# Performance work log

Measured on AMD Instinct MI355X. Metric: run time of the kernel, lower is better.

Reference implementation:

```python
import jax, jax.numpy as jnp
import numpy as np

NUM_EXPERTS = 8
IN_FEATURES = 1024
HIDDEN_FEATURES = 4096
OUT_FEATURES = 1024
TOKENS = 8192


def setup_inputs() -> dict:
    key = jax.random.key(0)
    k_x, k_idx, k_w1, k_w2, k_b1, k_b2 = jax.random.split(key, 6)
    x = jax.random.normal(k_x, (TOKENS, IN_FEATURES), dtype=jnp.float32)
    indices_s = jax.random.randint(k_idx, (TOKENS,), 0, NUM_EXPERTS, dtype=jnp.int64)
    # learned parameters (torch uses torch.rand; scaled for numeric sanity)
    weight1 = jax.random.normal(k_w1, (NUM_EXPERTS, IN_FEATURES, HIDDEN_FEATURES), dtype=jnp.float32) * 0.02
    weight2 = jax.random.normal(k_w2, (NUM_EXPERTS, HIDDEN_FEATURES, OUT_FEATURES), dtype=jnp.float32) * 0.02
    bias1 = jax.random.normal(k_b1, (NUM_EXPERTS, HIDDEN_FEATURES), dtype=jnp.float32) * 0.02
    bias2 = jax.random.normal(k_b2, (NUM_EXPERTS, IN_FEATURES), dtype=jnp.float32) * 0.02
    return {"x": x, "indices_s": indices_s, "weight1": weight1, "weight2": weight2, "bias1": bias1, "bias2": bias2}


def reference(x, indices_s, weight1, weight2, bias1, bias2):
    # Per-token expert MLP. Rather than gathering full weight matrices per
    # token (weight[indices_s] -> [T, in, hid], huge), loop over the small
    # fixed expert set and mask-combine. Math identical to the torch module.
    T = x.shape[0]
    num_experts = weight1.shape[0]
    out = jnp.zeros((T, weight2.shape[2]), dtype=x.dtype)
    for e in range(num_experts):
        mask = (indices_s == e)[:, None]  # [T, 1]
        h = jax.nn.gelu(x @ weight1[e] + bias1[e], approximate=False)  # [T, hid]
        y = h @ weight2[e] + bias2[e]  # [T, out]
        out = out + jnp.where(mask, y, jnp.zeros((), dtype=x.dtype))
    # original returns shape [T, 1, out] (x was unsqueezed)
    return out[:, None, :]
```

## Files before the change

kernel.cpp:

```cpp
#include <hip/hip_runtime.h>
#include <hip/hip_bf16.h>
#include <math.h>

#define TOKENS 8192
#define IN_F   1024
#define HID_F  4096
#define OUT_F  1024
#define NEXP   8
#define TSLOTS 40

typedef __attribute__((ext_vector_type(8))) short bf16x8;
typedef __attribute__((ext_vector_type(4))) float f32x4;
typedef __attribute__((ext_vector_type(8))) unsigned short u16x8;

__device__ __forceinline__ unsigned short f2bf(float f) {
    unsigned int u = __float_as_uint(f);
    u += 0x7fffu + ((u >> 16) & 1u);
    return (unsigned short)(u >> 16);
}

__device__ __forceinline__ void gload_lds16(const unsigned short* g, unsigned char* lds) {
    __builtin_amdgcn_global_load_lds(
        (const __attribute__((address_space(1))) void*)g,
        (__attribute__((address_space(3))) void*)lds, 16, 0, 0);
}

__global__ void sort_kernel(const int* __restrict__ idx, int* __restrict__ perm,
                            int* __restrict__ off, int* __restrict__ table) {
    __shared__ int cnt[NEXP];
    __shared__ int base[NEXP];
    const int tid = threadIdx.x, lane = tid & 63;
    if (tid < NEXP) cnt[tid] = 0;
    __syncthreads();
    for (int i = tid; i < TOKENS; i += 1024) {
        int e = idx[i];
#pragma unroll
        for (int ex = 0; ex < NEXP; ++ex) {
            unsigned long long m = __ballot(e == ex);
            if (lane == 0 && m) atomicAdd(&cnt[ex], __popcll(m));
        }
    }
    __syncthreads();
    if (tid == 0) {
        int s = 0;
        for (int e = 0; e < NEXP; ++e) { off[e] = s; base[e] = s; s += cnt[e]; }
        off[NEXP] = s;
        int t = 0;
        for (int e = 0; e < NEXP; ++e)
            for (int m0 = off[e]; m0 < off[e + 1]; m0 += 256)
                table[t++] = (e << 13) | m0;
        for (; t < TSLOTS; ++t) table[t] = -1;
    }
    __syncthreads();
    for (int i = tid; i < TOKENS; i += 1024) {
        int e = idx[i];
#pragma unroll
        for (int ex = 0; ex < NEXP; ++ex) {
            unsigned long long m = __ballot(e == ex);
            if (e == ex) {
                int lead = (int)__ffsll((long long)m) - 1;
                int pos = 0;
                if (lane == lead) pos = atomicAdd(&base[ex], __popcll(m));
                pos = __shfl(pos, lead);
                pos += __popcll(m & ((1ULL << lane) - 1ULL));
                perm[pos] = i;
            }
        }
    }
}

__global__ void gather_x(const float* __restrict__ x, const int* __restrict__ perm,
                         unsigned short* __restrict__ xg) {
    const int row = blockIdx.x, t = threadIdx.x;
    const int src = perm[row];
    float4 v = *(const float4*)(x + (size_t)src * IN_F + t * 4);
    unsigned long long pk =
        (unsigned long long)f2bf(v.x) |
        ((unsigned long long)f2bf(v.y) << 16) |
        ((unsigned long long)f2bf(v.z) << 32) |
        ((unsigned long long)f2bf(v.w) << 48);
    *(unsigned long long*)(xg + (size_t)row * IN_F + t * 4) = pk;
}

__global__ void transp(const float* __restrict__ in, unsigned short* __restrict__ out,
                       int R, int C) {
    __shared__ unsigned short T[64 * 65];
    const int e = blockIdx.z;
    const int r0 = blockIdx.y * 64, c0 = blockIdx.x * 64;
    const int tid = threadIdx.x;
    const int rr = tid >> 4, cc = tid & 15;
    const float* ip = in + ((size_t)e * R + r0) * C + c0;
#pragma unroll
    for (int p = 0; p < 4; ++p) {
        int r = p * 16 + rr;
        float4 v = *(const float4*)(ip + (size_t)r * C + cc * 4);
        T[(cc * 4 + 0) * 65 + r] = f2bf(v.x);
        T[(cc * 4 + 1) * 65 + r] = f2bf(v.y);
        T[(cc * 4 + 2) * 65 + r] = f2bf(v.z);
        T[(cc * 4 + 3) * 65 + r] = f2bf(v.w);
    }
    __syncthreads();
    unsigned short* op = out + ((size_t)e * C + c0) * R + r0;
    const int c = tid >> 2, ch = tid & 3;
    u16x8 a, b;
#pragma unroll
    for (int i = 0; i < 8; ++i) a[i] = T[c * 65 + ch * 16 + i];
#pragma unroll
    for (int i = 0; i < 8; ++i) b[i] = T[c * 65 + ch * 16 + 8 + i];
    *(u16x8*)(op + (size_t)c * R + ch * 16) = a;
    *(u16x8*)(op + (size_t)c * R + ch * 16 + 8) = b;
}

#define RD_A(RB, HALF) \
  _Pragma("unroll") for (int m_ = 0; m_ < 4; ++m_) { \
    const int row_ = wr * 128 + (HALF) * 64 + m_ * 16 + lr; \
    _Pragma("unroll") for (int kk_ = 0; kk_ < 2; ++kk_) \
      aR[m_][kk_] = *(const bf16x8*)((RB) + row_ * 128 + (((kk_ * 4 + hk) << 4) ^ xorc)); }

#define RD_B(RB, NH, DST) \
  _Pragma("unroll") for (int nn_ = 0; nn_ < 2; ++nn_) { \
    const int row_ = wc * 64 + ((NH) * 2 + nn_) * 16 + lr; \
    _Pragma("unroll") for (int kk_ = 0; kk_ < 2; ++kk_) \
      DST[nn_][kk_] = *(const bf16x8*)((RB) + 32768 + row_ * 128 + (((kk_ * 4 + hk) << 4) ^ xorc)); }

#define MFMA_Q(MH, NH, B) \
  __builtin_amdgcn_s_setprio(1); \
  _Pragma("unroll") for (int m_ = 0; m_ < 4; ++m_) \
    _Pragma("unroll") for (int nn_ = 0; nn_ < 2; ++nn_) \
      _Pragma("unroll") for (int kk_ = 0; kk_ < 2; ++kk_) \
        acc[(MH) * 4 + m_][(NH) * 2 + nn_] = __builtin_amdgcn_mfma_f32_16x16x32_bf16( \
            aR[m_][kk_], B[nn_][kk_], acc[(MH) * 4 + m_][(NH) * 2 + nn_], 0, 0, 0); \
  __builtin_amdgcn_s_setprio(0);

template<int K, int ND, bool GELU>
__launch_bounds__(512, 2)
__global__ void moe_gemm8p(const unsigned short* __restrict__ A,
                           const unsigned short* __restrict__ W,
                           const float* __restrict__ bias,
                           const int* __restrict__ perm,
                           const int* __restrict__ off,
                           const int* __restrict__ table,
                           void* __restrict__ outp) {
    const int nwg = (ND / 256) * TSLOTS;
    const int chunk = nwg >> 3;
    const int logical = ((int)blockIdx.x & 7) * chunk + ((int)blockIdx.x >> 3);
    const int nt = logical / TSLOTS;
    const int ts = logical - nt * TSLOTS;
    const int te = table[ts];
    if (te < 0) return;
    const int e  = te >> 13;
    const int m0 = te & 8191;
    const int sege = off[e + 1];
    const int n0 = nt * 256;

    __shared__ __align__(16) unsigned char L[131072];

    const int tid = threadIdx.x;
    const int wid = tid >> 6, lane = tid & 63;
    const int wr = wid >> 2, wc = wid & 3;
    const int lr = lane & 15, hk = lane >> 4;

    const unsigned short* We = W + (size_t)e * ND * K + (size_t)n0 * K;

    const int srow8 = lane >> 3;
    const int sch   = (lane & 7) ^ srow8;
    const unsigned short* aSrc[4];
    const unsigned short* wSrc[4];
#pragma unroll
    for (int cc = 0; cc < 4; ++cc) {
        int rt = cc * 64 + wid * 8 + srow8;
        int ga = m0 + rt; if (ga > TOKENS - 1) ga = TOKENS - 1;
        aSrc[cc] = A  + (size_t)ga * K + sch * 8;
        wSrc[cc] = We + (size_t)rt * K + sch * 8;
    }
    const int dstBase = wid * 1024;

    constexpr int NT = K / 64;

    auto stageH = [&](int tile, int h) {
        const int buf = (tile & 1) * 65536;
        const int op  = (h >> 1) * 32768;
        const int c0_ = (h & 1) * 2;
        const int ko  = tile * 64;
#pragma unroll
        for (int j = 0; j < 2; ++j) {
            int cc = c0_ + j;
            const unsigned short* s = (h < 2) ? (aSrc[cc] + ko) : (wSrc[cc] + ko);
            gload_lds16(s, L + buf + op + cc * 8192 + dstBase);
        }
    };

    f32x4 acc[8][4];
#pragma unroll
    for (int i = 0; i < 8; ++i)
#pragma unroll
        for (int j = 0; j < 4; ++j) acc[i][j] = (f32x4){0.f, 0.f, 0.f, 0.f};

    bf16x8 aR[4][2], b0R[2][2], b1R[2][2];
    const int xorc = (lr & 7) << 4;
    const unsigned char* rb0 = L;
    const unsigned char* rb1 = L + 65536;

    stageH(0, 0); stageH(0, 1); stageH(0, 2); stageH(0, 3);
    stageH(1, 0);
    asm volatile("s_waitcnt vmcnt(2)" ::: "memory");
    __builtin_amdgcn_s_barrier();
    __builtin_amdgcn_sched_barrier(0);

#pragma unroll 1
    for (int i = 0; i < NT / 2; ++i) {
        const int T1 = 2 * i + 1;
        const bool lastIt = (i == NT / 2 - 1);
        RD_A(rb0, 0); RD_B(rb0, 0, b0R);
        stageH(T1, 1);
        __builtin_amdgcn_s_barrier();
        MFMA_Q(0, 0, b0R);
        __builtin_amdgcn_s_barrier();
        RD_B(rb0, 1, b1R);
        stageH(T1, 2);
        __builtin_amdgcn_s_barrier();
        MFMA_Q(0, 1, b1R);
        __builtin_amdgcn_s_barrier();
        RD_A(rb0, 1);
        stageH(T1, 3);
        __builtin_amdgcn_s_barrier();
        MFMA_Q(1, 1, b1R);
        __builtin_amdgcn_s_barrier();
        RD_B(rb0, 0, b0R);
        if (!lastIt) stageH(T1 + 1, 0);
        __builtin_amdgcn_s_barrier();
        MFMA_Q(1, 0, b0R);
        if (lastIt) { asm volatile("s_waitcnt vmcnt(0)" ::: "memory"); }
        else        { asm volatile("s_waitcnt vmcnt(2)" ::: "memory"); }
        __builtin_amdgcn_s_barrier();
        __builtin_amdgcn_sched_barrier(0);
        RD_A(rb1, 0); RD_B(rb1, 0, b0R);
        if (!lastIt) stageH(T1 + 1, 1);
        __builtin_amdgcn_s_barrier();
        MFMA_Q(0, 0, b0R);
        __builtin_amdgcn_s_barrier();
        RD_B(rb1, 1, b1R);
        if (!lastIt) stageH(T1 + 1, 2);
        __builtin_amdgcn_s_barrier();
        MFMA_Q(0, 1, b1R);
        __builtin_amdgcn_s_barrier();
        RD_A(rb1, 1);
        if (!lastIt) stageH(T1 + 1, 3);
        __builtin_amdgcn_s_barrier();
        MFMA_Q(1, 1, b1R);
        __builtin_amdgcn_s_barrier();
        RD_B(rb1, 0, b0R);
        if (!lastIt) stageH(T1 + 2, 0);
        __builtin_amdgcn_s_barrier();
        MFMA_Q(1, 0, b0R);
        if (!lastIt) { asm volatile("s_waitcnt vmcnt(2)" ::: "memory"); }
        __builtin_amdgcn_s_barrier();
        __builtin_amdgcn_sched_barrier(0);
    }

    const float* be = bias + (size_t)e * ND + n0;
#pragma unroll
    for (int m = 0; m < 8; ++m) {
#pragma unroll
        for (int r = 0; r < 4; ++r) {
            int row = wr * 128 + m * 16 + hk * 4 + r;
            int grow = m0 + row;
            if (grow >= sege) continue;
            if constexpr (GELU) {
                unsigned short* h = (unsigned short*)outp;
                size_t base = (size_t)grow * ND + n0;
#pragma unroll
                for (int n = 0; n < 4; ++n) {
                    int col = wc * 64 + n * 16 + lr;
                    float v = acc[m][n][r] + be[col];
                    float u = v * (0.7978845608f + 0.0356774081f * v * v);
                    float g = v / (1.0f + __expf(-2.0f * u));
                    h[base + col] = f2bf(g);
                }
            } else {
                float* out = (float*)outp;
                int tok = perm[grow];
                size_t base = (size_t)tok * ND + n0;
#pragma unroll
                for (int n = 0; n < 4; ++n) {
                    int col = wc * 64 + n * 16 + lr;
                    out[base + col] = acc[m][n][r] + be[col];
                }
            }
        }
    }
}

extern "C" void kernel_launch(void* const* d_in, const int* in_sizes, int n_in,
                              void* d_out, int out_size, void* d_ws, size_t ws_size,
                              hipStream_t stream) {
    const float* x   = (const float*)d_in[0];
    const int*   idx = (const int*)d_in[1];
    const float* w1  = (const float*)d_in[2];
    const float* w2  = (const float*)d_in[3];
    const float* b1  = (const float*)d_in[4];
    const float* b2  = (const float*)d_in[5];
    float* out = (float*)d_out;

    int* perm  = (int*)d_ws;
    int* off   = perm + TOKENS;
    int* table = off + 16;
    unsigned short* xg = (unsigned short*)((char*)d_ws + 65536);
    unsigned short* h  = xg + (size_t)TOKENS * IN_F;
    unsigned short* wt = h + (size_t)TOKENS * HID_F;

    hipLaunchKernelGGL(sort_kernel, dim3(1), dim3(1024), 0, stream, idx, perm, off, table);
    hipLaunchKernelGGL(gather_x, dim3(TOKENS), dim3(256), 0, stream, x, perm, xg);

    hipLaunchKernelGGL(transp, dim3(HID_F / 64, IN_F / 64, NEXP), dim3(256), 0, stream,
                       w1, wt, IN_F, HID_F);
    hipLaunchKernelGGL((moe_gemm8p<IN_F, HID_F, true>), dim3((HID_F / 256) * TSLOTS), dim3(512),
                       0, stream, xg, wt, b1, perm, off, table, (void*)h);

    hipLaunchKernelGGL(transp, dim3(OUT_F / 64, HID_F / 64, NEXP), dim3(256), 0, stream,
                       w2, wt, HID_F, OUT_F);
    hipLaunchKernelGGL((moe_gemm8p<HID_F, OUT_F, false>), dim3((OUT_F / 256) * TSLOTS), dim3(512),
                       0, stream, h, wt, b2, perm, off, table, (void*)out);
}
```

Baseline: 338.0 us.

## Split-K the second expert GEMM in two with a bf16 partial-sum reduction

The second GEMM (K=4096, N=1024) launches only 160 workgroups, so its K dimension is now split in two, doubling the workgroup count to fill the GPU. The first K-half adds bias and writes fp32 output directly. The second half writes bf16 partials into the reused xg buffer, and a new reduce kernel adds them into the output by token. The redundant reload of the B fragment before the last MFMA quarter is also removed. The split costs an extra kernel launch, extra partial-sum memory traffic, and bf16 rounding of half of the accumulation.

```diff
diff --git a/kernel.cpp b/kernel.cpp
--- a/kernel.cpp
+++ b/kernel.cpp
@@ -111,6 +111,25 @@
     *(u16x8*)(op + (size_t)c * R + ch * 16 + 8) = b;
 }
 
+__global__ void reduce_partial(const unsigned short* __restrict__ P,
+                               const int* __restrict__ perm,
+                               float* __restrict__ out) {
+    const int grow = blockIdx.x, t = threadIdx.x;
+    const int tok = perm[grow];
+    u16x8 p = *(const u16x8*)(P + (size_t)grow * OUT_F + t * 8);
+    float* o = out + (size_t)tok * OUT_F + t * 8;
+    float4 lo = *(float4*)o, hi = *(float4*)(o + 4);
+    lo.x += __uint_as_float((unsigned)p[0] << 16);
+    lo.y += __uint_as_float((unsigned)p[1] << 16);
+    lo.z += __uint_as_float((unsigned)p[2] << 16);
+    lo.w += __uint_as_float((unsigned)p[3] << 16);
+    hi.x += __uint_as_float((unsigned)p[4] << 16);
+    hi.y += __uint_as_float((unsigned)p[5] << 16);
+    hi.z += __uint_as_float((unsigned)p[6] << 16);
+    hi.w += __uint_as_float((unsigned)p[7] << 16);
+    *(float4*)o = lo; *(float4*)(o + 4) = hi;
+}
+
 #define RD_A(RB, HALF) \
   _Pragma("unroll") for (int m_ = 0; m_ < 4; ++m_) { \
     const int row_ = wr * 128 + (HALF) * 64 + m_ * 16 + lr; \
@@ -132,7 +151,7 @@
             aR[m_][kk_], B[nn_][kk_], acc[(MH) * 4 + m_][(NH) * 2 + nn_], 0, 0, 0); \
   __builtin_amdgcn_s_setprio(0);
 
-template<int K, int ND, bool GELU>
+template<int KROW, int NT_, int ND, int NSPLIT, bool GELU>
 __launch_bounds__(512, 2)
 __global__ void moe_gemm8p(const unsigned short* __restrict__ A,
                            const unsigned short* __restrict__ W,
@@ -140,18 +159,23 @@
                            const int* __restrict__ perm,
                            const int* __restrict__ off,
                            const int* __restrict__ table,
-                           void* __restrict__ outp) {
-    const int nwg = (ND / 256) * TSLOTS;
+                           void* __restrict__ outp,
+                           unsigned short* __restrict__ Ppart) {
+    const int nper = (ND / 256) * TSLOTS;
+    const int nwg = nper * NSPLIT;
     const int chunk = nwg >> 3;
     const int logical = ((int)blockIdx.x & 7) * chunk + ((int)blockIdx.x >> 3);
-    const int nt = logical / TSLOTS;
-    const int ts = logical - nt * TSLOTS;
+    const int ks  = logical / nper;
+    const int rem = logical - ks * nper;
+    const int nt = rem / TSLOTS;
+    const int ts = rem - nt * TSLOTS;
     const int te = table[ts];
     if (te < 0) return;
     const int e  = te >> 13;
     const int m0 = te & 8191;
     const int sege = off[e + 1];
     const int n0 = nt * 256;
+    const int k_off = ks * (NT_ * 64);
 
     __shared__ __align__(16) unsigned char L[131072];
 
@@ -160,7 +184,7 @@
     const int wr = wid >> 2, wc = wid & 3;
     const int lr = lane & 15, hk = lane >> 4;
 
-    const unsigned short* We = W + (size_t)e * ND * K + (size_t)n0 * K;
+    const unsigned short* We = W + (size_t)e * ND * KROW + (size_t)n0 * KROW;
 
     const int srow8 = lane >> 3;
     const int sch   = (lane & 7) ^ srow8;
@@ -170,12 +194,10 @@
     for (int cc = 0; cc < 4; ++cc) {
         int rt = cc * 64 + wid * 8 + srow8;
         int ga = m0 + rt; if (ga > TOKENS - 1) ga = TOKENS - 1;
-        aSrc[cc] = A  + (size_t)ga * K + sch * 8;
-        wSrc[cc] = We + (size_t)rt * K + sch * 8;
+        aSrc[cc] = A  + (size_t)ga * KROW + k_off + sch * 8;
+        wSrc[cc] = We + (size_t)rt * KROW + k_off + sch * 8;
     }
     const int dstBase = wid * 1024;
-
-    constexpr int NT = K / 64;
 
     auto stageH = [&](int tile, int h) {
         const int buf = (tile & 1) * 65536;
@@ -208,9 +230,9 @@
     __builtin_amdgcn_sched_barrier(0);
 
 #pragma unroll 1
-    for (int i = 0; i < NT / 2; ++i) {
+    for (int i = 0; i < NT_ / 2; ++i) {
         const int T1 = 2 * i + 1;
-        const bool lastIt = (i == NT / 2 - 1);
+        const bool lastIt = (i == NT_ / 2 - 1);
         RD_A(rb0, 0); RD_B(rb0, 0, b0R);
         stageH(T1, 1);
         __builtin_amdgcn_s_barrier();
@@ -226,7 +248,6 @@
         __builtin_amdgcn_s_barrier();
         MFMA_Q(1, 1, b1R);
         __builtin_amdgcn_s_barrier();
-        RD_B(rb0, 0, b0R);
         if (!lastIt) stageH(T1 + 1, 0);
         __builtin_amdgcn_s_barrier();
         MFMA_Q(1, 0, b0R);
@@ -249,7 +270,6 @@
         __builtin_amdgcn_s_barrier();
         MFMA_Q(1, 1, b1R);
         __builtin_amdgcn_s_barrier();
-        RD_B(rb1, 0, b0R);
         if (!lastIt) stageH(T1 + 2, 0);
         __builtin_amdgcn_s_barrier();
         MFMA_Q(1, 0, b0R);
@@ -278,13 +298,22 @@
                     h[base + col] = f2bf(g);
                 }
             } else {
-                float* out = (float*)outp;
-                int tok = perm[grow];
-                size_t base = (size_t)tok * ND + n0;
-#pragma unroll
-                for (int n = 0; n < 4; ++n) {
-                    int col = wc * 64 + n * 16 + lr;
-                    out[base + col] = acc[m][n][r] + be[col];
+                if (ks == 0) {
+                    float* out = (float*)outp;
+                    int tok = perm[grow];
+                    size_t base = (size_t)tok * ND + n0;
+#pragma unroll
+                    for (int n = 0; n < 4; ++n) {
+                        int col = wc * 64 + n * 16 + lr;
+                        out[base + col] = acc[m][n][r] + be[col];
+                    }
+                } else {
+                    size_t base = (size_t)grow * ND + n0;
+#pragma unroll
+                    for (int n = 0; n < 4; ++n) {
+                        int col = wc * 64 + n * 16 + lr;
+                        Ppart[base + col] = f2bf(acc[m][n][r]);
+                    }
                 }
             }
         }
@@ -308,17 +337,21 @@
     unsigned short* xg = (unsigned short*)((char*)d_ws + 65536);
     unsigned short* h  = xg + (size_t)TOKENS * IN_F;
     unsigned short* wt = h + (size_t)TOKENS * HID_F;
+    unsigned short* P  = xg;
 
     hipLaunchKernelGGL(sort_kernel, dim3(1), dim3(1024), 0, stream, idx, perm, off, table);
     hipLaunchKernelGGL(gather_x, dim3(TOKENS), dim3(256), 0, stream, x, perm, xg);
 
     hipLaunchKernelGGL(transp, dim3(HID_F / 64, IN_F / 64, NEXP), dim3(256), 0, stream,
                        w1, wt, IN_F, HID_F);
-    hipLaunchKernelGGL((moe_gemm8p<IN_F, HID_F, true>), dim3((HID_F / 256) * TSLOTS), dim3(512),
-                       0, stream, xg, wt, b1, perm, off, table, (void*)h);
+    hipLaunchKernelGGL((moe_gemm8p<IN_F, 16, HID_F, 1, true>),
+                       dim3((HID_F / 256) * TSLOTS), dim3(512),
+                       0, stream, xg, wt, b1, perm, off, table, (void*)h, (unsigned short*)0);
 
     hipLaunchKernelGGL(transp, dim3(OUT_F / 64, HID_F / 64, NEXP), dim3(256), 0, stream,
                        w2, wt, HID_F, OUT_F);
-    hipLaunchKernelGGL((moe_gemm8p<HID_F, OUT_F, false>), dim3((OUT_F / 256) * TSLOTS), dim3(512),
-                       0, stream, h, wt, b2, perm, off, table, (void*)out);
-}
+    hipLaunchKernelGGL((moe_gemm8p<HID_F, 32, OUT_F, 2, false>),
+                       dim3((OUT_F / 256) * TSLOTS * 2), dim3(512),
+                       0, stream, h, wt, b2, perm, off, table, (void*)out, P);
+    hipLaunchKernelGGL(reduce_partial, dim3(TOKENS), dim3(128), 0, stream, P, perm, out);
+}
```

Result: slower. 359.8 us (+6.5%).

## Fuse gather with W1 transpose and overlap W2 transpose inside first GEMM

Applied to the files above, without the earlier changes.

Merges the token gather/bf16 cast and the W1 transpose into one launch. When the workspace is large enough, the W2 transpose runs as extra blocks of the first expert GEMM, writing to a separate buffer so it can overlap with GEMM work instead of running as its own launch. It also drops a redundant reload of the B fragment in the GEMM main loop, reusing registers that already hold it. This cuts launch count and serialization, at the cost of extra workspace and transpose blocks competing for CUs with the GEMM.

```diff
diff --git a/kernel.cpp b/kernel.cpp
--- a/kernel.cpp
+++ b/kernel.cpp
@@ -69,26 +69,12 @@
     }
 }
 
-__global__ void gather_x(const float* __restrict__ x, const int* __restrict__ perm,
-                         unsigned short* __restrict__ xg) {
-    const int row = blockIdx.x, t = threadIdx.x;
-    const int src = perm[row];
-    float4 v = *(const float4*)(x + (size_t)src * IN_F + t * 4);
-    unsigned long long pk =
-        (unsigned long long)f2bf(v.x) |
-        ((unsigned long long)f2bf(v.y) << 16) |
-        ((unsigned long long)f2bf(v.z) << 32) |
-        ((unsigned long long)f2bf(v.w) << 48);
-    *(unsigned long long*)(xg + (size_t)row * IN_F + t * 4) = pk;
-}
-
-__global__ void transp(const float* __restrict__ in, unsigned short* __restrict__ out,
-                       int R, int C) {
-    __shared__ unsigned short T[64 * 65];
-    const int e = blockIdx.z;
-    const int r0 = blockIdx.y * 64, c0 = blockIdx.x * 64;
-    const int tid = threadIdx.x;
-    const int rr = tid >> 4, cc = tid & 15;
+__device__ __forceinline__ void transp_tile(const float* __restrict__ in,
+                                            unsigned short* __restrict__ out,
+                                            int R, int C, int e, int by, int bx,
+                                            unsigned short* T, int st) {
+    const int r0 = by * 64, c0 = bx * 64;
+    const int rr = st >> 4, cc = st & 15;
     const float* ip = in + ((size_t)e * R + r0) * C + c0;
 #pragma unroll
     for (int p = 0; p < 4; ++p) {
@@ -101,7 +87,7 @@
     }
     __syncthreads();
     unsigned short* op = out + ((size_t)e * C + c0) * R + r0;
-    const int c = tid >> 2, ch = tid & 3;
+    const int c = st >> 2, ch = st & 3;
     u16x8 a, b;
 #pragma unroll
     for (int i = 0; i < 8; ++i) a[i] = T[c * 65 + ch * 16 + i];
@@ -109,6 +95,34 @@
     for (int i = 0; i < 8; ++i) b[i] = T[c * 65 + ch * 16 + 8 + i];
     *(u16x8*)(op + (size_t)c * R + ch * 16) = a;
     *(u16x8*)(op + (size_t)c * R + ch * 16 + 8) = b;
+}
+
+__global__ void transp(const float* __restrict__ in, unsigned short* __restrict__ out,
+                       int R, int C) {
+    __shared__ unsigned short T[64 * 65];
+    transp_tile(in, out, R, C, blockIdx.z, blockIdx.y, blockIdx.x, T, threadIdx.x);
+}
+
+__global__ void fused_pre(const float* __restrict__ x, const int* __restrict__ perm,
+                          unsigned short* __restrict__ xg,
+                          const float* __restrict__ w1, unsigned short* __restrict__ w1t) {
+    __shared__ unsigned short T[64 * 65];
+    const int bid = blockIdx.x, t = threadIdx.x;
+    if (bid < TOKENS) {
+        const int src = perm[bid];
+        float4 v = *(const float4*)(x + (size_t)src * IN_F + t * 4);
+        unsigned long long pk =
+            (unsigned long long)f2bf(v.x) |
+            ((unsigned long long)f2bf(v.y) << 16) |
+            ((unsigned long long)f2bf(v.z) << 32) |
+            ((unsigned long long)f2bf(v.w) << 48);
+        *(unsigned long long*)(xg + (size_t)bid * IN_F + t * 4) = pk;
+        return;
+    }
+    const int id = bid - TOKENS;
+    const int e = id >> 10, rem = id & 1023;
+    const int by = rem >> 6, bx = rem & 63;
+    transp_tile(w1, w1t, IN_F, HID_F, e, by, bx, T, t);
 }
 
 #define RD_A(RB, HALF) \
@@ -140,8 +154,24 @@
                            const int* __restrict__ perm,
                            const int* __restrict__ off,
                            const int* __restrict__ table,
-                           void* __restrict__ outp) {
+                           void* __restrict__ outp,
+                           const float* __restrict__ w2src,
+                           unsigned short* __restrict__ w2t) {
     const int nwg = (ND / 256) * TSLOTS;
+
+    __shared__ __align__(16) unsigned char L[131072];
+    const int tid = threadIdx.x;
+
+    if ((int)blockIdx.x >= nwg) {
+        const int sub = tid >> 8, st = tid & 255;
+        const int id2 = ((int)blockIdx.x - nwg) * 2 + sub;
+        const int e = id2 >> 10, rem = id2 & 1023;
+        const int by = rem >> 4, bx = rem & 15;
+        unsigned short* T = (unsigned short*)(L + sub * 8448);
+        transp_tile(w2src, w2t, HID_F, OUT_F, e, by, bx, T, st);
+        return;
+    }
+
     const int chunk = nwg >> 3;
     const int logical = ((int)blockIdx.x & 7) * chunk + ((int)blockIdx.x >> 3);
     const int nt = logical / TSLOTS;
@@ -153,9 +183,6 @@
     const int sege = off[e + 1];
     const int n0 = nt * 256;
 
-    __shared__ __align__(16) unsigned char L[131072];
-
-    const int tid = threadIdx.x;
     const int wid = tid >> 6, lane = tid & 63;
     const int wr = wid >> 2, wc = wid & 3;
     const int lr = lane & 15, hk = lane >> 4;
@@ -226,7 +253,6 @@
         __builtin_amdgcn_s_barrier();
         MFMA_Q(1, 1, b1R);
         __builtin_amdgcn_s_barrier();
-        RD_B(rb0, 0, b0R);
         if (!lastIt) stageH(T1 + 1, 0);
         __builtin_amdgcn_s_barrier();
         MFMA_Q(1, 0, b0R);
@@ -249,7 +275,6 @@
         __builtin_amdgcn_s_barrier();
         MFMA_Q(1, 1, b1R);
         __builtin_amdgcn_s_barrier();
-        RD_B(rb1, 0, b0R);
         if (!lastIt) stageH(T1 + 2, 0);
         __builtin_amdgcn_s_barrier();
         MFMA_Q(1, 0, b0R);
@@ -305,20 +330,38 @@
     int* perm  = (int*)d_ws;
     int* off   = perm + TOKENS;
     int* table = off + 16;
-    unsigned short* xg = (unsigned short*)((char*)d_ws + 65536);
-    unsigned short* h  = xg + (size_t)TOKENS * IN_F;
-    unsigned short* wt = h + (size_t)TOKENS * HID_F;
+    unsigned short* xg  = (unsigned short*)((char*)d_ws + 65536);
+    unsigned short* h   = xg + (size_t)TOKENS * IN_F;
+    unsigned short* w1t = h + (size_t)TOKENS * HID_F;
+    unsigned short* w2t = w1t + (size_t)NEXP * IN_F * HID_F;
+    const size_t need_fused = 65536
+        + (size_t)TOKENS * IN_F * 2
+        + (size_t)TOKENS * HID_F * 2
+        + (size_t)NEXP * IN_F * HID_F * 2 * 2;
+    const bool fused = (ws_size >= need_fused);
 
     hipLaunchKernelGGL(sort_kernel, dim3(1), dim3(1024), 0, stream, idx, perm, off, table);
-    hipLaunchKernelGGL(gather_x, dim3(TOKENS), dim3(256), 0, stream, x, perm, xg);
-
-    hipLaunchKernelGGL(transp, dim3(HID_F / 64, IN_F / 64, NEXP), dim3(256), 0, stream,
-                       w1, wt, IN_F, HID_F);
-    hipLaunchKernelGGL((moe_gemm8p<IN_F, HID_F, true>), dim3((HID_F / 256) * TSLOTS), dim3(512),
-                       0, stream, xg, wt, b1, perm, off, table, (void*)h);
-
-    hipLaunchKernelGGL(transp, dim3(OUT_F / 64, HID_F / 64, NEXP), dim3(256), 0, stream,
-                       w2, wt, HID_F, OUT_F);
-    hipLaunchKernelGGL((moe_gemm8p<HID_F, OUT_F, false>), dim3((OUT_F / 256) * TSLOTS), dim3(512),
-                       0, stream, h, wt, b2, perm, off, table, (void*)out);
-}
+    hipLaunchKernelGGL(fused_pre, dim3(TOKENS + NEXP * (IN_F / 64) * (HID_F / 64)),
+                       dim3(256), 0, stream, x, perm, xg, w1, w1t);
+
+    const int g1 = (HID_F / 256) * TSLOTS;
+    const int t2 = NEXP * (OUT_F / 64) * (HID_F / 64) / 2;
+    if (fused) {
+        hipLaunchKernelGGL((moe_gemm8p<IN_F, HID_F, true>), dim3(g1 + t2), dim3(512),
+                           0, stream, xg, w1t, b1, perm, off, table, (void*)h, w2, w2t);
+        hipLaunchKernelGGL((moe_gemm8p<HID_F, OUT_F, false>),
+                           dim3((OUT_F / 256) * TSLOTS), dim3(512),
+                           0, stream, h, w2t, b2, perm, off, table, (void*)out,
+                           (const float*)nullptr, (unsigned short*)nullptr);
+    } else {
+        hipLaunchKernelGGL((moe_gemm8p<IN_F, HID_F, true>), dim3(g1), dim3(512),
+                           0, stream, xg, w1t, b1, perm, off, table, (void*)h,
+                           (const float*)nullptr, (unsigned short*)nullptr);
+        hipLaunchKernelGGL(transp, dim3(OUT_F / 64, HID_F / 64, NEXP), dim3(256), 0, stream,
+                           w2, w1t, HID_F, OUT_F);
+        hipLaunchKernelGGL((moe_gemm8p<HID_F, OUT_F, false>),
+                           dim3((OUT_F / 256) * TSLOTS), dim3(512),
+                           0, stream, h, w1t, b2, perm, off, table, (void*)out,
+                           (const float*)nullptr, (unsigned short*)nullptr);
+    }
+}
```

Measured after the change: 320.0 us. -5.3%, faster.
